# Kernel optimization log

Measured on AMD Instinct MI355X. Metric: run time of the kernel, lower is better.

The kernel has to match this reference:

```python
import jax, jax.numpy as jnp
import numpy as np

C = 256
HEADS = 8
HD = C // HEADS
SCALE = HD ** -0.5


def conv1x1(x, W, b):
    # x: [B,C_in,H,W], W: [C_out,C_in], b: [C_out]
    return jnp.einsum('oc,bchw->bohw', W, x) + b[None, :, None, None]


def setup_inputs() -> dict:
    key = jax.random.key(0)
    ks = jax.random.split(key, 12)
    B, H, Wd = 2, 48, 48
    s = C ** -0.5
    return {
        'x': jax.random.normal(ks[0], (B, C, H, Wd), jnp.float32),
        'uncertainty': jax.random.uniform(ks[1], (B, 1, H, Wd), jnp.float32),
        'Wq': jax.random.normal(ks[2], (C, C), jnp.float32) * s,
        'bq': jnp.zeros((C,), jnp.float32),
        'Wk': jax.random.normal(ks[3], (C, C), jnp.float32) * s,
        'bk': jnp.zeros((C,), jnp.float32),
        'Wv': jax.random.normal(ks[4], (C, C), jnp.float32) * s,
        'bv': jnp.zeros((C,), jnp.float32),
        'Wg': jax.random.normal(ks[5], (C, 1), jnp.float32),
        'bg': jnp.zeros((C,), jnp.float32),
        'Wo': jax.random.normal(ks[6], (C, C), jnp.float32) * s,
        'bo': jnp.zeros((C,), jnp.float32),
    }


def reference(x, uncertainty, Wq, bq, Wk, bk, Wv, bv, Wg, bg, Wo, bo):
    B, _, H, Wd = x.shape
    N = H * Wd
    # uncertainty gate (1x1 conv from 1 channel to C channels)
    uw = conv1x1(uncertainty, Wg, bg)            # [B,C,H,W]
    gated_x = x * (1.0 - uw)
    q = conv1x1(gated_x, Wq, bq).reshape(B, HEADS, HD, N)
    k = conv1x1(gated_x, Wk, bk).reshape(B, HEADS, HD, N)
    v = conv1x1(x, Wv, bv).reshape(B, HEADS, HD, N)
    # scores: [B,h,N,N] (query tokens n, key tokens m)
    scores = jnp.einsum('bhdn,bhdm->bhnm', q, k) * SCALE
    u_flat = uncertainty.reshape(B, 1, 1, N)      # mask over key axis
    scores = scores * (1.0 - u_flat)
    attn = jax.nn.softmax(scores, axis=-1)
    out = jnp.einsum('bhnm,bhdm->bhdn', attn, v)  # [B,h,hd,N]
    out = out.reshape(B, C, H, Wd)
    out = conv1x1(out, Wo, bo)
    return out + x
```

## Files before the change

### kernel.cpp

```cpp
#include <hip/hip_runtime.h>
#include <hip/hip_bf16.h>

typedef float f32x4 __attribute__((ext_vector_type(4)));
typedef __bf16 bf16x8 __attribute__((ext_vector_type(8)));
typedef __bf16 bf16x4 __attribute__((ext_vector_type(4)));
typedef short s16x4 __attribute__((ext_vector_type(4)));

constexpr int C = 256;
constexpr int N = 2304;
constexpr int T = 2 * N;

#if __has_builtin(__builtin_amdgcn_exp2f)
#define EXP2F(x) __builtin_amdgcn_exp2f(x)
#else
#define EXP2F(x) exp2f(x)
#endif

__device__ __forceinline__ bf16x8 load_bf8(const __bf16* p) {
    return *reinterpret_cast<const bf16x8*>(p);
}

__device__ __forceinline__ f32x4 mfma32(bf16x8 a, bf16x8 b, f32x4 c) {
    return __builtin_amdgcn_mfma_f32_16x16x32_bf16(a, b, c, 0, 0, 0);
}

#if __has_builtin(__builtin_amdgcn_mfma_f32_16x16x16bf16_1k)
__device__ __forceinline__ f32x4 mfma16(bf16x4 a, bf16x4 b, f32x4 c) {
    return __builtin_amdgcn_mfma_f32_16x16x16bf16_1k(
        __builtin_bit_cast(s16x4, a), __builtin_bit_cast(s16x4, b), c, 0, 0, 0);
}
#else
__device__ __forceinline__ f32x4 mfma16(bf16x4 a, bf16x4 b, f32x4 c) {
    f32x4 d;
    asm volatile("v_mfma_f32_16x16x16_bf16 %0, %1, %2, %3"
                 : "=v"(d) : "v"(a), "v"(b), "v"(c));
    return d;
}
#endif

__device__ __forceinline__ void gload_lds16(const __bf16* g, __bf16* l) {
    __builtin_amdgcn_global_load_lds(
        (const __attribute__((address_space(1))) void*)g,
        (__attribute__((address_space(3))) void*)l, 16, 0, 0);
}

#define VMCNT0() asm volatile("s_waitcnt vmcnt(0)" ::: "memory")

__global__ void wconv_kernel(const float* __restrict__ Wq, const float* __restrict__ Wk,
                             const float* __restrict__ Wv, const float* __restrict__ Wo,
                             __bf16* __restrict__ Wb) {
    const float* srcs[4] = {Wq, Wk, Wv, Wo};
    int m = blockIdx.x >> 6;
    int idx = (blockIdx.x & 63) * 256 + threadIdx.x;
    float4 v = reinterpret_cast<const float4*>(srcs[m])[idx];
    bf16x4 o = { (__bf16)v.x, (__bf16)v.y, (__bf16)v.z, (__bf16)v.w };
    reinterpret_cast<bf16x4*>(Wb + m * 65536)[idx] = o;
}

__global__ void prep_kernel(const float* __restrict__ x, const float* __restrict__ u,
                            const float* __restrict__ Wg, const float* __restrict__ bg,
                            __bf16* __restrict__ xT, __bf16* __restrict__ gxT) {
    __shared__ float tile[32][65];
    int b = blockIdx.z, c0 = blockIdx.y * 32, n0 = blockIdx.x * 64;
    int t = threadIdx.x;
    const float* xp = x + (b * C + c0) * N + n0;
    #pragma unroll
    for (int r = 0; r < 8; ++r) {
        int cl = r * 4 + (t >> 6);
        int nl = t & 63;
        tile[cl][nl] = xp[cl * N + nl];
    }
    __syncthreads();
    int cq = (t & 7) * 4;
    #pragma unroll
    for (int it = 0; it < 2; ++it) {
        int nl = it * 32 + (t >> 3);
        float uv = u[b * N + n0 + nl];
        bf16x4 xo, go;
        #pragma unroll
        for (int j = 0; j < 4; ++j) {
            int c = c0 + cq + j;
            float xv = tile[cq + j][nl];
            float gate = 1.0f - (Wg[c] * uv + bg[c]);
            xo[j] = (__bf16)xv;
            go[j] = (__bf16)(xv * gate);
        }
        int tok = b * N + n0 + nl;
        *reinterpret_cast<bf16x4*>(xT + (long)tok * C + c0 + cq) = xo;
        *reinterpret_cast<bf16x4*>(gxT + (long)tok * C + c0 + cq) = go;
    }
}

__global__ __launch_bounds__(256) void qkv_kernel(const __bf16* __restrict__ Wb,
    const __bf16* __restrict__ xT, const __bf16* __restrict__ gxT,
    const float* __restrict__ bq, const float* __restrict__ bk, const float* __restrict__ bv,
    const float* __restrict__ u,
    __bf16* __restrict__ Q, __bf16* __restrict__ K, __bf16* __restrict__ V) {
    int proj = blockIdx.z;
    int o0 = blockIdx.y * 64;
    int t0 = blockIdx.x * 32;
    int wave = threadIdx.x >> 6, lane = threadIdx.x & 63;
    int g = lane >> 4, r = lane & 15;
    int ow = o0 + wave * 16;
    const __bf16* W = Wb + proj * 65536;
    const __bf16* inp = (proj == 2) ? xT : gxT;
    f32x4 acc[2] = {};
    for (int k = 0; k < 8; ++k) {
        bf16x8 a = load_bf8(W + (ow + r) * C + k * 32 + g * 8);
        #pragma unroll
        for (int tb = 0; tb < 2; ++tb) {
            bf16x8 bfr = load_bf8(inp + (long)(t0 + tb * 16 + r) * C + k * 32 + g * 8);
            acc[tb] = mfma32(a, bfr, acc[tb]);
        }
    }
    const float* bias = (proj == 0) ? bq : (proj == 1) ? bk : bv;
    float bvw[4];
    #pragma unroll
    for (int i = 0; i < 4; ++i) bvw[i] = bias[ow + g * 4 + i];
    int h = ow >> 5, d0 = (ow & 31) + g * 4;
    const float SC = 0.17677669529663687f * 1.4426950408889634f;
    #pragma unroll
    for (int tb = 0; tb < 2; ++tb) {
        int t = t0 + tb * 16 + r;
        int b = t / N, n = t % N;
        if (proj == 2) {
            #pragma unroll
            for (int i = 0; i < 4; ++i)
                V[((long)(b * 8 + h) * 32 + d0 + i) * N + n] = (__bf16)(acc[tb][i] + bvw[i]);
        } else {
            bf16x4 outv;
            if (proj == 1) {
                float scale = SC * (1.0f - u[t]);
                #pragma unroll
                for (int i = 0; i < 4; ++i) outv[i] = (__bf16)((acc[tb][i] + bvw[i]) * scale);
            } else {
                #pragma unroll
                for (int i = 0; i < 4; ++i) outv[i] = (__bf16)(acc[tb][i] + bvw[i]);
            }
            __bf16* dst = (proj == 0) ? Q : K;
            *reinterpret_cast<bf16x4*>(dst + ((long)(b * 8 + h) * N + n) * 32 + d0) = outv;
        }
    }
}

__global__ __launch_bounds__(256) void attn_kernel(const __bf16* __restrict__ Q,
    const __bf16* __restrict__ K, const __bf16* __restrict__ V,
    __bf16* __restrict__ aoT) {
    __shared__ __bf16 sMem[16384];
    int id = blockIdx.x;
    int xcd = id & 7, j = id >> 3;
    int bh = xcd + 8 * (j / 72);
    int qblk = j % 72;
    int tid = threadIdx.x;
    int wave = tid >> 6, lane = tid & 63;
    int g = lane >> 4, r = lane & 15;
    int q0 = qblk * 32;
    const __bf16* Qg = Q + (long)bh * N * 32;
    const __bf16* Kg = K + (long)bh * N * 32 + (long)wave * 576 * 32;
    const __bf16* Vg = V + (long)bh * 32 * N + wave * 576;
    bf16x8 qf0 = load_bf8(Qg + (q0 + r) * 32 + g * 8);
    bf16x8 qf1 = load_bf8(Qg + (q0 + 16 + r) * 32 + g * 8);
    int l0 = lane ^ ((lane >> 3) & 7);
    const __bf16* kS = Kg + (l0 >> 2) * 32 + (l0 & 3) * 8;
    const __bf16* vS = Vg + (long)(l0 >> 2) * N + (l0 & 3) * 8;
    __bf16* kB = sMem + wave * 4096;
    __bf16* vB = kB + 2048;
    auto STAGE = [&](long m0, int buf) {
        gload_lds16(kS + m0 * 32,       kB + buf * 1024);
        gload_lds16(kS + m0 * 32 + 512, kB + buf * 1024 + 512);
        gload_lds16(vS + m0,            vB + buf * 1024);
        gload_lds16(vS + 16 * N + m0,   vB + buf * 1024 + 512);
    };
    int key = (r >> 1) & 7;
    int pk0 = ((r * 4 + g) ^ key) * 8;
    int pk1 = (((16 + r) * 4 + g) ^ key) * 8;
    int pv00 = ((r * 4 + 0 + (g >> 1)) ^ key) * 8 + (g & 1) * 4;
    int pv01 = (((16 + r) * 4 + 0 + (g >> 1)) ^ key) * 8 + (g & 1) * 4;
    int pv10 = ((r * 4 + 2 + (g >> 1)) ^ key) * 8 + (g & 1) * 4;
    int pv11 = (((16 + r) * 4 + 2 + (g >> 1)) ^ key) * 8 + (g & 1) * 4;
    bf16x4 onesv;
    #pragma unroll
    for (int i = 0; i < 4; ++i) onesv[i] = (__bf16)1.0f;
    f32x4 oa00 = {}, oa01 = {}, oa10 = {}, oa11 = {};
    f32x4 oal0 = {}, oal1 = {};
    STAGE(0, 0);
    for (int t = 0; t < 18; ++t) {
        VMCNT0();
        const __bf16* kb = kB + (t & 1) * 1024;
        const __bf16* vb = vB + (t & 1) * 1024;
        if (t < 17) STAGE((long)(t + 1) * 32, (t & 1) ^ 1);
        bf16x8 kc0 = load_bf8(kb + pk0);
        bf16x8 kc1 = load_bf8(kb + pk1);
        bf16x4 vf00 = *reinterpret_cast<const bf16x4*>(vb + pv00);
        bf16x4 vf01 = *reinterpret_cast<const bf16x4*>(vb + pv01);
        bf16x4 vf10 = *reinterpret_cast<const bf16x4*>(vb + pv10);
        bf16x4 vf11 = *reinterpret_cast<const bf16x4*>(vb + pv11);
        f32x4 z = {};
        __builtin_amdgcn_s_setprio(1);
        f32x4 s00 = mfma32(kc0, qf0, z);
        f32x4 s01 = mfma32(kc1, qf0, z);
        f32x4 s10 = mfma32(kc0, qf1, z);
        f32x4 s11 = mfma32(kc1, qf1, z);
        __builtin_amdgcn_s_setprio(0);
        bf16x4 pa00, pa01, pa10, pa11;
        #pragma unroll
        for (int i = 0; i < 4; ++i) pa00[i] = (__bf16)EXP2F(s00[i]);
        #pragma unroll
        for (int i = 0; i < 4; ++i) pa01[i] = (__bf16)EXP2F(s01[i]);
        #pragma unroll
        for (int i = 0; i < 4; ++i) pa10[i] = (__bf16)EXP2F(s10[i]);
        #pragma unroll
        for (int i = 0; i < 4; ++i) pa11[i] = (__bf16)EXP2F(s11[i]);
        __builtin_amdgcn_s_setprio(1);
        oa00 = mfma16(vf00, pa00, oa00);
        oa01 = mfma16(vf01, pa00, oa01);
        oal0 = mfma16(onesv, pa00, oal0);
        oa00 = mfma16(vf10, pa01, oa00);
        oa01 = mfma16(vf11, pa01, oa01);
        oal0 = mfma16(onesv, pa01, oal0);
        oa10 = mfma16(vf00, pa10, oa10);
        oa11 = mfma16(vf01, pa10, oa11);
        oal1 = mfma16(onesv, pa10, oal1);
        oa10 = mfma16(vf10, pa11, oa10);
        oa11 = mfma16(vf11, pa11, oa11);
        oal1 = mfma16(onesv, pa11, oal1);
        __builtin_amdgcn_s_setprio(0);
    }
    __syncthreads();
    float* F = reinterpret_cast<float*>(sMem);
    float* D = F + 4096;
    *reinterpret_cast<f32x4*>(F + wave * 1024 + r * 32 + g * 4) = oa00;
    *reinterpret_cast<f32x4*>(F + wave * 1024 + r * 32 + 16 + g * 4) = oa01;
    *reinterpret_cast<f32x4*>(F + wave * 1024 + 512 + r * 32 + g * 4) = oa10;
    *reinterpret_cast<f32x4*>(F + wave * 1024 + 512 + r * 32 + 16 + g * 4) = oa11;
    if (g == 0) {
        D[wave * 32 + r] = oal0[0];
        D[wave * 32 + 16 + r] = oal1[0];
    }
    __syncthreads();
    {
        int q = tid >> 3;
        int d4 = (tid & 7) * 4;
        int qt = q >> 4, qq = q & 15;
        int base = qt * 512 + qq * 32 + d4;
        f32x4 sum = *reinterpret_cast<f32x4*>(F + base) +
                    *reinterpret_cast<f32x4*>(F + 1024 + base) +
                    *reinterpret_cast<f32x4*>(F + 2048 + base) +
                    *reinterpret_cast<f32x4*>(F + 3072 + base);
        float l = D[qt * 16 + qq] + D[32 + qt * 16 + qq] +
                  D[64 + qt * 16 + qq] + D[96 + qt * 16 + qq];
        float inv = 1.0f / l;
        bf16x4 ov;
        #pragma unroll
        for (int i = 0; i < 4; ++i) ov[i] = (__bf16)(sum[i] * inv);
        int b = bh >> 3, h = bh & 7;
        *reinterpret_cast<bf16x4*>(aoT + (long)(b * N + q0 + q) * C + h * 32 + d4) = ov;
    }
}

__global__ __launch_bounds__(256) void outp_kernel(const __bf16* __restrict__ Wb,
    const __bf16* __restrict__ aoT, const float* __restrict__ bo,
    const float* __restrict__ x, float* __restrict__ out) {
    int o0 = blockIdx.y * 64;
    int t0 = blockIdx.x * 16;
    int wave = threadIdx.x >> 6, lane = threadIdx.x & 63;
    int g = lane >> 4, r = lane & 15;
    int ow = o0 + wave * 16;
    const __bf16* W = Wb + 3 * 65536;
    f32x4 acc = {};
    for (int k = 0; k < 8; ++k) {
        bf16x8 a = load_bf8(W + (ow + r) * C + k * 32 + g * 8);
        bf16x8 bfr = load_bf8(aoT + (long)(t0 + r) * C + k * 32 + g * 8);
        acc = mfma32(a, bfr, acc);
    }
    float bvw[4];
    #pragma unroll
    for (int i = 0; i < 4; ++i) bvw[i] = bo[ow + g * 4 + i];
    int t = t0 + r;
    int b = t / N, n = t % N;
    #pragma unroll
    for (int i = 0; i < 4; ++i) {
        long idx = ((long)b * C + ow + g * 4 + i) * N + n;
        out[idx] = acc[i] + bvw[i] + x[idx];
    }
}

extern "C" void kernel_launch(void* const* d_in, const int* in_sizes, int n_in,
                              void* d_out, int out_size, void* d_ws, size_t ws_size,
                              hipStream_t stream) {
    const float* x  = (const float*)d_in[0];
    const float* u  = (const float*)d_in[1];
    const float* Wq = (const float*)d_in[2];
    const float* bq = (const float*)d_in[3];
    const float* Wk = (const float*)d_in[4];
    const float* bk = (const float*)d_in[5];
    const float* Wv = (const float*)d_in[6];
    const float* bv = (const float*)d_in[7];
    const float* Wg = (const float*)d_in[8];
    const float* bg = (const float*)d_in[9];
    const float* Wo = (const float*)d_in[10];
    const float* bo = (const float*)d_in[11];
    float* out = (float*)d_out;

    char* ws = (char*)d_ws;
    size_t off = 0;
    auto alloc = [&](size_t bytes) {
        char* p = ws + off;
        off += (bytes + 255) & ~(size_t)255;
        return p;
    };
    __bf16* Wb  = (__bf16*)alloc((size_t)4 * 65536 * 2);
    __bf16* xT  = (__bf16*)alloc((size_t)T * C * 2);
    __bf16* gxT = (__bf16*)alloc((size_t)T * C * 2);
    __bf16* Qb  = (__bf16*)alloc((size_t)16 * N * 32 * 2);
    __bf16* Kb  = (__bf16*)alloc((size_t)16 * N * 32 * 2);
    __bf16* Vb  = (__bf16*)alloc((size_t)16 * N * 32 * 2);
    __bf16* aoT = (__bf16*)alloc((size_t)T * C * 2);

    wconv_kernel<<<256, 256, 0, stream>>>(Wq, Wk, Wv, Wo, Wb);
    prep_kernel<<<dim3(36, 8, 2), 256, 0, stream>>>(x, u, Wg, bg, xT, gxT);
    qkv_kernel<<<dim3(144, 4, 3), 256, 0, stream>>>(Wb, xT, gxT, bq, bk, bv, u, Qb, Kb, Vb);
    attn_kernel<<<1152, 256, 0, stream>>>(Qb, Kb, Vb, aoT);
    outp_kernel<<<dim3(288, 4), 256, 0, stream>>>(Wb, aoT, bo, x, out);
}
```

Before: 77.73 us.

## Split attention keys across eight waves and compute row sums on VALU

The attention kernel now launches 512 threads and splits the key range across 8 waves instead of 4. Each wave stages 16-key tiles, which halves its per-wave LDS buffers and its per-iteration MFMA work. The softmax denominator is now accumulated in registers from the exp values and reduced with lane shuffles, replacing the extra ones-vector MFMAs. The partial-output LDS stores and reads are XOR-swizzled to cut bank conflicts. In exchange, the final cross-wave reduction covers twice as many partials and each wave iterates over smaller tiles with more frequent waits.

```diff
diff --git a/kernel.cpp b/kernel.cpp
--- a/kernel.cpp
+++ b/kernel.cpp
@@ -143,10 +143,10 @@
     }
 }
 
-__global__ __launch_bounds__(256) void attn_kernel(const __bf16* __restrict__ Q,
+__global__ __launch_bounds__(512) void attn_kernel(const __bf16* __restrict__ Q,
     const __bf16* __restrict__ K, const __bf16* __restrict__ V,
     __bf16* __restrict__ aoT) {
-    __shared__ __bf16 sMem[16384];
+    __shared__ __bf16 sMem[16896];
     int id = blockIdx.x;
     int xcd = id & 7, j = id >> 3;
     int bh = xcd + 8 * (j / 72);
@@ -156,105 +156,102 @@
     int g = lane >> 4, r = lane & 15;
     int q0 = qblk * 32;
     const __bf16* Qg = Q + (long)bh * N * 32;
-    const __bf16* Kg = K + (long)bh * N * 32 + (long)wave * 576 * 32;
-    const __bf16* Vg = V + (long)bh * 32 * N + wave * 576;
+    const __bf16* Kg = K + (long)bh * N * 32 + (long)wave * 288 * 32;
+    const __bf16* Vg = V + (long)bh * 32 * N + wave * 288;
     bf16x8 qf0 = load_bf8(Qg + (q0 + r) * 32 + g * 8);
     bf16x8 qf1 = load_bf8(Qg + (q0 + 16 + r) * 32 + g * 8);
     int l0 = lane ^ ((lane >> 3) & 7);
     const __bf16* kS = Kg + (l0 >> 2) * 32 + (l0 & 3) * 8;
-    const __bf16* vS = Vg + (long)(l0 >> 2) * N + (l0 & 3) * 8;
-    __bf16* kB = sMem + wave * 4096;
-    __bf16* vB = kB + 2048;
+    const __bf16* vS = Vg + (long)(l0 >> 1) * N + (l0 & 1) * 8;
+    __bf16* kB = sMem + wave * 2048;
+    __bf16* vB = kB + 1024;
     auto STAGE = [&](long m0, int buf) {
-        gload_lds16(kS + m0 * 32,       kB + buf * 1024);
-        gload_lds16(kS + m0 * 32 + 512, kB + buf * 1024 + 512);
-        gload_lds16(vS + m0,            vB + buf * 1024);
-        gload_lds16(vS + 16 * N + m0,   vB + buf * 1024 + 512);
+        gload_lds16(kS + m0 * 32, kB + buf * 512);
+        gload_lds16(vS + m0,      vB + buf * 512);
     };
-    int key = (r >> 1) & 7;
-    int pk0 = ((r * 4 + g) ^ key) * 8;
-    int pk1 = (((16 + r) * 4 + g) ^ key) * 8;
-    int pv00 = ((r * 4 + 0 + (g >> 1)) ^ key) * 8 + (g & 1) * 4;
-    int pv01 = (((16 + r) * 4 + 0 + (g >> 1)) ^ key) * 8 + (g & 1) * 4;
-    int pv10 = ((r * 4 + 2 + (g >> 1)) ^ key) * 8 + (g & 1) * 4;
-    int pv11 = (((16 + r) * 4 + 2 + (g >> 1)) ^ key) * 8 + (g & 1) * 4;
-    bf16x4 onesv;
-    #pragma unroll
-    for (int i = 0; i < 4; ++i) onesv[i] = (__bf16)1.0f;
+    int ck = r * 4 + g;
+    int pk = (ck ^ ((ck >> 3) & 7)) * 8;
+    int cv0 = r * 2 + (g >> 1);
+    int cv1 = 32 + cv0;
+    int pv0 = (cv0 ^ ((cv0 >> 3) & 7)) * 8 + (g & 1) * 4;
+    int pv1 = (cv1 ^ ((cv1 >> 3) & 7)) * 8 + (g & 1) * 4;
     f32x4 oa00 = {}, oa01 = {}, oa10 = {}, oa11 = {};
-    f32x4 oal0 = {}, oal1 = {};
+    float lr0 = 0.0f, lr1 = 0.0f;
     STAGE(0, 0);
     for (int t = 0; t < 18; ++t) {
         VMCNT0();
-        const __bf16* kb = kB + (t & 1) * 1024;
-        const __bf16* vb = vB + (t & 1) * 1024;
-        if (t < 17) STAGE((long)(t + 1) * 32, (t & 1) ^ 1);
-        bf16x8 kc0 = load_bf8(kb + pk0);
-        bf16x8 kc1 = load_bf8(kb + pk1);
-        bf16x4 vf00 = *reinterpret_cast<const bf16x4*>(vb + pv00);
-        bf16x4 vf01 = *reinterpret_cast<const bf16x4*>(vb + pv01);
-        bf16x4 vf10 = *reinterpret_cast<const bf16x4*>(vb + pv10);
-        bf16x4 vf11 = *reinterpret_cast<const bf16x4*>(vb + pv11);
+        const __bf16* kb = kB + (t & 1) * 512;
+        const __bf16* vb = vB + (t & 1) * 512;
+        if (t < 17) STAGE((long)(t + 1) * 16, (t & 1) ^ 1);
+        bf16x8 kc = load_bf8(kb + pk);
+        bf16x4 vf0 = *reinterpret_cast<const bf16x4*>(vb + pv0);
+        bf16x4 vf1 = *reinterpret_cast<const bf16x4*>(vb + pv1);
         f32x4 z = {};
         __builtin_amdgcn_s_setprio(1);
-        f32x4 s00 = mfma32(kc0, qf0, z);
-        f32x4 s01 = mfma32(kc1, qf0, z);
-        f32x4 s10 = mfma32(kc0, qf1, z);
-        f32x4 s11 = mfma32(kc1, qf1, z);
+        f32x4 s0 = mfma32(kc, qf0, z);
+        f32x4 s1 = mfma32(kc, qf1, z);
         __builtin_amdgcn_s_setprio(0);
-        bf16x4 pa00, pa01, pa10, pa11;
-        #pragma unroll
-        for (int i = 0; i < 4; ++i) pa00[i] = (__bf16)EXP2F(s00[i]);
-        #pragma unroll
-        for (int i = 0; i < 4; ++i) pa01[i] = (__bf16)EXP2F(s01[i]);
-        #pragma unroll
-        for (int i = 0; i < 4; ++i) pa10[i] = (__bf16)EXP2F(s10[i]);
-        #pragma unroll
-        for (int i = 0; i < 4; ++i) pa11[i] = (__bf16)EXP2F(s11[i]);
+        bf16x4 pa0, pa1;
+        #pragma unroll
+        for (int i = 0; i < 4; ++i) {
+            float p = EXP2F(s0[i]);
+            lr0 += p;
+            pa0[i] = (__bf16)p;
+        }
+        #pragma unroll
+        for (int i = 0; i < 4; ++i) {
+            float p = EXP2F(s1[i]);
+            lr1 += p;
+            pa1[i] = (__bf16)p;
+        }
         __builtin_amdgcn_s_setprio(1);
-        oa00 = mfma16(vf00, pa00, oa00);
-        oa01 = mfma16(vf01, pa00, oa01);
-        oal0 = mfma16(onesv, pa00, oal0);
-        oa00 = mfma16(vf10, pa01, oa00);
-        oa01 = mfma16(vf11, pa01, oa01);
-        oal0 = mfma16(onesv, pa01, oal0);
-        oa10 = mfma16(vf00, pa10, oa10);
-        oa11 = mfma16(vf01, pa10, oa11);
-        oal1 = mfma16(onesv, pa10, oal1);
-        oa10 = mfma16(vf10, pa11, oa10);
-        oa11 = mfma16(vf11, pa11, oa11);
-        oal1 = mfma16(onesv, pa11, oal1);
+        oa00 = mfma16(vf0, pa0, oa00);
+        oa01 = mfma16(vf1, pa0, oa01);
+        oa10 = mfma16(vf0, pa1, oa10);
+        oa11 = mfma16(vf1, pa1, oa11);
         __builtin_amdgcn_s_setprio(0);
     }
+    float lt0 = lr0;
+    lt0 += __shfl_xor(lt0, 16, 64);
+    lt0 += __shfl_xor(lt0, 32, 64);
+    float lt1 = lr1;
+    lt1 += __shfl_xor(lt1, 16, 64);
+    lt1 += __shfl_xor(lt1, 32, 64);
     __syncthreads();
     float* F = reinterpret_cast<float*>(sMem);
-    float* D = F + 4096;
-    *reinterpret_cast<f32x4*>(F + wave * 1024 + r * 32 + g * 4) = oa00;
-    *reinterpret_cast<f32x4*>(F + wave * 1024 + r * 32 + 16 + g * 4) = oa01;
-    *reinterpret_cast<f32x4*>(F + wave * 1024 + 512 + r * 32 + g * 4) = oa10;
-    *reinterpret_cast<f32x4*>(F + wave * 1024 + 512 + r * 32 + 16 + g * 4) = oa11;
+    float* D = F + 8192;
+    int fb = wave * 1024 + r * 32;
+    int sg = g ^ (r & 7);
+    *reinterpret_cast<f32x4*>(F + fb + sg * 4) = oa00;
+    *reinterpret_cast<f32x4*>(F + fb + (sg ^ 4) * 4) = oa01;
+    *reinterpret_cast<f32x4*>(F + fb + 512 + sg * 4) = oa10;
+    *reinterpret_cast<f32x4*>(F + fb + 512 + (sg ^ 4) * 4) = oa11;
+    if (lane == 0) {
+        D[wave * 32 + r] = lt0;
+    }
     if (g == 0) {
-        D[wave * 32 + r] = oal0[0];
-        D[wave * 32 + 16 + r] = oal1[0];
+        D[wave * 32 + r] = lt0;
+        D[wave * 32 + 16 + r] = lt1;
     }
     __syncthreads();
-    {
+    if (tid < 256) {
         int q = tid >> 3;
-        int d4 = (tid & 7) * 4;
+        int dg = tid & 7;
         int qt = q >> 4, qq = q & 15;
-        int base = qt * 512 + qq * 32 + d4;
-        f32x4 sum = *reinterpret_cast<f32x4*>(F + base) +
-                    *reinterpret_cast<f32x4*>(F + 1024 + base) +
-                    *reinterpret_cast<f32x4*>(F + 2048 + base) +
-                    *reinterpret_cast<f32x4*>(F + 3072 + base);
-        float l = D[qt * 16 + qq] + D[32 + qt * 16 + qq] +
-                  D[64 + qt * 16 + qq] + D[96 + qt * 16 + qq];
+        int off = qt * 512 + qq * 32 + (dg ^ (qq & 7)) * 4;
+        f32x4 sum = {};
+        float l = 0.0f;
+        #pragma unroll
+        for (int w = 0; w < 8; ++w) {
+            sum += *reinterpret_cast<const f32x4*>(F + w * 1024 + off);
+            l += D[w * 32 + qt * 16 + qq];
+        }
         float inv = 1.0f / l;
         bf16x4 ov;
         #pragma unroll
         for (int i = 0; i < 4; ++i) ov[i] = (__bf16)(sum[i] * inv);
         int b = bh >> 3, h = bh & 7;
-        *reinterpret_cast<bf16x4*>(aoT + (long)(b * N + q0 + q) * C + h * 32 + d4) = ov;
+        *reinterpret_cast<bf16x4*>(aoT + (long)(b * N + q0 + q) * C + h * 32 + dg * 4) = ov;
     }
 }
 
@@ -320,6 +317,6 @@
     wconv_kernel<<<256, 256, 0, stream>>>(Wq, Wk, Wv, Wo, Wb);
     prep_kernel<<<dim3(36, 8, 2), 256, 0, stream>>>(x, u, Wg, bg, xT, gxT);
     qkv_kernel<<<dim3(144, 4, 3), 256, 0, stream>>>(Wb, xT, gxT, bq, bk, bv, u, Qb, Kb, Vb);
-    attn_kernel<<<1152, 256, 0, stream>>>(Qb, Kb, Vb, aoT);
+    attn_kernel<<<1152, 512, 0, stream>>>(Qb, Kb, Vb, aoT);
     outp_kernel<<<dim3(288, 4), 256, 0, stream>>>(Wb, aoT, bo, x, out);
 }
```

After: 77.95 us. About the same (+0.3%).
